# Performance work log

Measured on AMD Instinct MI355X. Metric: run time of the kernel, lower is better.

## Reference

```python
import jax, jax.numpy as jnp
import numpy as np

NEG_INF = -1e30  # large negative in place of -inf for masked scores (fp32-safe)


def setup_inputs() -> dict:
    key = jax.random.key(0)
    kq, kk, kv, km = jax.random.split(key, 4)
    B, H, S, D = 2, 16, 2048, 64
    query = jax.random.normal(kq, (B, H, S, D), dtype=jnp.float32)
    k = jax.random.normal(kk, (B, H, S, D), dtype=jnp.float32)
    v = jax.random.normal(kv, (B, H, S, D), dtype=jnp.float32)
    mask = jax.random.randint(km, (B, H, S, S), 0, 2, dtype=jnp.int32)
    return {"query": query, "key": k, "value": v, "mask": mask}


def reference(query, key, value, mask):
    # Online-softmax chunked attention is mathematically exact softmax attention;
    # we compute the equivalent masked softmax attention in one fused expression.
    d_k = query.shape[-1]
    scale = 1.0 / np.sqrt(d_k).astype(np.float32)
    # scores: [B, H, Sq, Sk]
    scores = jnp.einsum('bhqd,bhkd->bhqk', query, key) * scale
    scores = jnp.where(mask == 0, NEG_INF, scores)
    attn = jax.nn.softmax(scores, axis=-1)
    out = jnp.einsum('bhqk,bhkd->bhqd', attn, value)
    return out
```

## Files before the change

kernel.cpp:

```cpp
#include <hip/hip_runtime.h>


typedef __attribute__((ext_vector_type(8))) short bf16x8;
typedef __attribute__((ext_vector_type(4))) float f32x4;

#define S_LEN 2048
#define D_DIM 64
#define QT 64
#define KT 64
#define LROW 72
#define NEG_BIG (-1e30f)

__device__ __forceinline__ short f2bf(float f) {
    union { float f; unsigned u; } v; v.f = f;
    unsigned r = v.u + 0x7fffu + ((v.u >> 16) & 1u);
    return (short)(r >> 16);
}

__global__ __launch_bounds__(256, 4)
void fa_fwd(const float* __restrict__ Q, const float* __restrict__ K,
            const float* __restrict__ V, const int* __restrict__ M,
            float* __restrict__ O) {
    __shared__ __align__(16) short Kb[KT * LROW];
    __shared__ __align__(16) short Vt[D_DIM * LROW];
    __shared__ __align__(16) short Pw[4 * 16 * LROW];

    const int tid  = threadIdx.x;
    const int lane = tid & 63;
    const int w    = tid >> 6;
    const int quad = lane >> 4;
    const int c    = lane & 15;

    const int bid = blockIdx.x;
    const int x = bid & 7, y = bid >> 3;
    const int bh = x * 4 + (y >> 5);
    const int q0 = (y & 31) * QT;

    const float* qrow = Q + ((size_t)(bh * S_LEN + q0 + w * 16 + c)) * D_DIM;
    bf16x8 qfrag[2];
#pragma unroll
    for (int ks = 0; ks < 2; ++ks) {
        const float* p = qrow + ks * 32 + quad * 8;
        float4 a = *(const float4*)p;
        float4 b = *(const float4*)(p + 4);
        bf16x8 f;
        f[0]=f2bf(a.x); f[1]=f2bf(a.y); f[2]=f2bf(a.z); f[3]=f2bf(a.w);
        f[4]=f2bf(b.x); f[5]=f2bf(b.y); f[6]=f2bf(b.z); f[7]=f2bf(b.w);
        qfrag[ks] = f;
    }

    f32x4 acco[4];
    float m_i[4], l_i[4];
#pragma unroll
    for (int r = 0; r < 4; ++r) {
        m_i[r] = NEG_BIG; l_i[r] = 0.f;
        acco[r][0]=0.f; acco[r][1]=0.f; acco[r][2]=0.f; acco[r][3]=0.f;
    }

    const int kkt = tid >> 2;
    const int dsb = (tid & 3) * 16;
    const int kp  = (tid & 31) * 2;
    const int dbv = (tid >> 5) * 8;
    const float* Kbase = K + (size_t)bh * S_LEN * D_DIM;
    const float* Vbase = V + (size_t)bh * S_LEN * D_DIM;
    const int* mbase = M + ((size_t)(bh * S_LEN + q0 + w * 16 + quad * 4)) * S_LEN + c;
    short* pw = &Pw[w * 16 * LROW];

    for (int k0 = 0; k0 < S_LEN; k0 += KT) {
        int mv[4][4];
#pragma unroll
        for (int reg = 0; reg < 4; ++reg)
#pragma unroll
            for (int nb = 0; nb < 4; ++nb)
                mv[reg][nb] = mbase[(size_t)reg * S_LEN + k0 + nb * 16];

        {
            const float* kr = Kbase + (size_t)(k0 + kkt) * D_DIM + dsb;
            float4 a = *(const float4*)kr;
            float4 b = *(const float4*)(kr + 4);
            float4 cc = *(const float4*)(kr + 8);
            float4 d = *(const float4*)(kr + 12);
            short* dst = &Kb[kkt * LROW + dsb];
            bf16x8 f0, f1;
            f0[0]=f2bf(a.x);  f0[1]=f2bf(a.y);  f0[2]=f2bf(a.z);  f0[3]=f2bf(a.w);
            f0[4]=f2bf(b.x);  f0[5]=f2bf(b.y);  f0[6]=f2bf(b.z);  f0[7]=f2bf(b.w);
            f1[0]=f2bf(cc.x); f1[1]=f2bf(cc.y); f1[2]=f2bf(cc.z); f1[3]=f2bf(cc.w);
            f1[4]=f2bf(d.x);  f1[5]=f2bf(d.y);  f1[6]=f2bf(d.z);  f1[7]=f2bf(d.w);
            *(bf16x8*)dst = f0;
            *(bf16x8*)(dst + 8) = f1;
        }
        {
            const float* v0 = Vbase + (size_t)(k0 + kp) * D_DIM + dbv;
            const float* v1 = v0 + D_DIM;
            float4 a0 = *(const float4*)v0, a1 = *(const float4*)(v0 + 4);
            float4 b0 = *(const float4*)v1, b1 = *(const float4*)(v1 + 4);
            float av[8] = {a0.x,a0.y,a0.z,a0.w,a1.x,a1.y,a1.z,a1.w};
            float bv[8] = {b0.x,b0.y,b0.z,b0.w,b1.x,b1.y,b1.z,b1.w};
#pragma unroll
            for (int i = 0; i < 8; ++i) {
                unsigned pr = (unsigned short)f2bf(av[i]) |
                              ((unsigned)(unsigned short)f2bf(bv[i]) << 16);
                *(unsigned*)&Vt[(dbv + i) * LROW + kp] = pr;
            }
        }
        __syncthreads();

        f32x4 accs[4];
#pragma unroll
        for (int nb = 0; nb < 4; ++nb) { accs[nb][0]=0.f; accs[nb][1]=0.f; accs[nb][2]=0.f; accs[nb][3]=0.f; }
#pragma unroll
        for (int nb = 0; nb < 4; ++nb)
#pragma unroll
            for (int ks = 0; ks < 2; ++ks) {
                bf16x8 bfr = *(const bf16x8*)&Kb[(nb * 16 + c) * LROW + ks * 32 + quad * 8];
                accs[nb] = __builtin_amdgcn_mfma_f32_16x16x32_bf16(qfrag[ks], bfr, accs[nb], 0, 0, 0);
            }

        float s[4][4], rmax[4];
#pragma unroll
        for (int reg = 0; reg < 4; ++reg) {
            float rm = NEG_BIG;
#pragma unroll
            for (int nb = 0; nb < 4; ++nb) {
                float sv = accs[nb][reg] * 0.125f;
                sv = (mv[reg][nb] != 0) ? sv : NEG_BIG;
                s[reg][nb] = sv;
                rm = fmaxf(rm, sv);
            }
            rm = fmaxf(rm, __shfl_xor(rm, 1));
            rm = fmaxf(rm, __shfl_xor(rm, 2));
            rm = fmaxf(rm, __shfl_xor(rm, 4));
            rm = fmaxf(rm, __shfl_xor(rm, 8));
            rmax[reg] = rm;
        }
        float alpha[4];
#pragma unroll
        for (int reg = 0; reg < 4; ++reg) {
            float mn = fmaxf(m_i[reg], rmax[reg]);
            alpha[reg] = __expf(m_i[reg] - mn);
            m_i[reg] = mn;
        }
        float p[4][4];
#pragma unroll
        for (int reg = 0; reg < 4; ++reg) {
            float rs = 0.f;
#pragma unroll
            for (int nb = 0; nb < 4; ++nb) {
                float pv = __expf(s[reg][nb] - m_i[reg]);
                p[reg][nb] = pv;
                rs += pv;
            }
            rs += __shfl_xor(rs, 1);
            rs += __shfl_xor(rs, 2);
            rs += __shfl_xor(rs, 4);
            rs += __shfl_xor(rs, 8);
            l_i[reg] = l_i[reg] * alpha[reg] + rs;
        }
#pragma unroll
        for (int db = 0; db < 4; ++db)
#pragma unroll
            for (int reg = 0; reg < 4; ++reg)
                acco[db][reg] *= alpha[reg];

#pragma unroll
        for (int reg = 0; reg < 4; ++reg)
#pragma unroll
            for (int nb = 0; nb < 4; ++nb)
                pw[(quad * 4 + reg) * LROW + nb * 16 + c] = f2bf(p[reg][nb]);

        bf16x8 pfr0 = *(const bf16x8*)&pw[c * LROW + quad * 8];
        bf16x8 pfr1 = *(const bf16x8*)&pw[c * LROW + 32 + quad * 8];

#pragma unroll
        for (int db = 0; db < 4; ++db) {
            bf16x8 v0f = *(const bf16x8*)&Vt[(db * 16 + c) * LROW + quad * 8];
            acco[db] = __builtin_amdgcn_mfma_f32_16x16x32_bf16(pfr0, v0f, acco[db], 0, 0, 0);
            bf16x8 v1f = *(const bf16x8*)&Vt[(db * 16 + c) * LROW + 32 + quad * 8];
            acco[db] = __builtin_amdgcn_mfma_f32_16x16x32_bf16(pfr1, v1f, acco[db], 0, 0, 0);
        }
        __syncthreads();
    }

    float* orow = O + ((size_t)(bh * S_LEN + q0 + w * 16 + quad * 4)) * D_DIM + c;
#pragma unroll
    for (int reg = 0; reg < 4; ++reg) {
        float inv = 1.0f / l_i[reg];
#pragma unroll
        for (int db = 0; db < 4; ++db)
            orow[(size_t)reg * D_DIM + db * 16] = acco[db][reg] * inv;
    }
}

extern "C" void kernel_launch(void* const* d_in, const int* in_sizes, int n_in,
                              void* d_out, int out_size, void* d_ws, size_t ws_size,
                              hipStream_t stream) {
    const float* Q = (const float*)d_in[0];
    const float* K = (const float*)d_in[1];
    const float* V = (const float*)d_in[2];
    const int*   M = (const int*)d_in[3];
    float* O = (float*)d_out;
    hipLaunchKernelGGL(fa_fwd, dim3(1024), dim3(256), 0, stream, Q, K, V, M, O);
}
```

Measured before the change: 794.2 us.

## Pre-pack Q/K/V into MFMA fragment layout and drop online max rescaling

Adds three pre-pass kernels that convert Q (pre-scaled by 1/8), K and V into bf16 in the exact per-lane MFMA fragment order, stored in workspace. The main kernel then loads K/V tiles straight into LDS with double-buffered global_load_lds while prefetching the mask for the next tile, so per-tile conversion and transposition disappear. It also drops the running max and rescaling and exponentiates raw scores directly, with masked entries set to zero. That removes the shuffles and alpha multiplies but risks overflow for large scores, and a row whose mask is all zero now divides by zero instead of giving the reference's uniform average.

```diff
diff --git a/kernel.cpp b/kernel.cpp
--- a/kernel.cpp
+++ b/kernel.cpp
@@ -6,10 +6,8 @@
 
 #define S_LEN 2048
 #define D_DIM 64
-#define QT 64
-#define KT 64
-#define LROW 72
-#define NEG_BIG (-1e30f)
+#define NT 32
+#define PP 72
 
 __device__ __forceinline__ short f2bf(float f) {
     union { float f; unsigned u; } v; v.f = f;
@@ -17,13 +15,86 @@
     return (short)(r >> 16);
 }
 
-__global__ __launch_bounds__(256, 4)
-void fa_fwd(const float* __restrict__ Q, const float* __restrict__ K,
-            const float* __restrict__ V, const int* __restrict__ M,
-            float* __restrict__ O) {
-    __shared__ __align__(16) short Kb[KT * LROW];
-    __shared__ __align__(16) short Vt[D_DIM * LROW];
-    __shared__ __align__(16) short Pw[4 * 16 * LROW];
+__device__ __forceinline__ bf16x8 cvt8(float4 a, float4 b, float s) {
+    bf16x8 f;
+    f[0]=f2bf(a.x*s); f[1]=f2bf(a.y*s); f[2]=f2bf(a.z*s); f[3]=f2bf(a.w*s);
+    f[4]=f2bf(b.x*s); f[5]=f2bf(b.y*s); f[6]=f2bf(b.z*s); f[7]=f2bf(b.w*s);
+    return f;
+}
+
+__global__ __launch_bounds__(256)
+void pack_q(const float* __restrict__ Q, short* __restrict__ Qw) {
+    const int bh = blockIdx.x, qt = blockIdx.y;
+    for (int ci = threadIdx.x; ci < 512; ci += 256) {
+        int w = ci >> 7, ks = (ci >> 6) & 1, lane = ci & 63;
+        int quad = lane >> 4, c = lane & 15;
+        int row = qt * 64 + w * 16 + c;
+        int d0 = ks * 32 + quad * 8;
+        const float* src = Q + ((size_t)(bh * S_LEN + row)) * D_DIM + d0;
+        float4 a = *(const float4*)src;
+        float4 b = *(const float4*)(src + 4);
+        *(bf16x8*)(Qw + ((size_t)(bh * 32 + qt) * 512 + ci) * 8) = cvt8(a, b, 0.125f);
+    }
+}
+
+__global__ __launch_bounds__(256)
+void pack_k(const float* __restrict__ K, short* __restrict__ Kw) {
+    const int bh = blockIdx.x, t = blockIdx.y;
+    for (int ci = threadIdx.x; ci < 512; ci += 256) {
+        int fb = ci >> 6, lane = ci & 63;
+        int nb = fb >> 1, ks = fb & 1;
+        int quad = lane >> 4, c = lane & 15;
+        int key = t * 64 + c * 4 + nb;
+        int d0 = ks * 32 + quad * 8;
+        const float* src = K + ((size_t)(bh * S_LEN + key)) * D_DIM + d0;
+        float4 a = *(const float4*)src;
+        float4 b = *(const float4*)(src + 4);
+        *(bf16x8*)(Kw + ((size_t)(bh * 32 + t) * 512 + ci) * 8) = cvt8(a, b, 1.0f);
+    }
+}
+
+__global__ __launch_bounds__(256)
+void pack_v(const float* __restrict__ V, short* __restrict__ Vw) {
+    __shared__ float vt[64][65];
+    const int bh = blockIdx.x, t = blockIdx.y;
+    {
+        int key = threadIdx.x >> 2, d0 = (threadIdx.x & 3) * 16;
+        const float* src = V + ((size_t)(bh * S_LEN + t * 64 + key)) * D_DIM + d0;
+        float4 a = *(const float4*)src;
+        float4 b = *(const float4*)(src + 4);
+        float4 cc = *(const float4*)(src + 8);
+        float4 d = *(const float4*)(src + 12);
+        float* dst = &vt[key][d0];
+        dst[0]=a.x; dst[1]=a.y; dst[2]=a.z; dst[3]=a.w;
+        dst[4]=b.x; dst[5]=b.y; dst[6]=b.z; dst[7]=b.w;
+        dst[8]=cc.x; dst[9]=cc.y; dst[10]=cc.z; dst[11]=cc.w;
+        dst[12]=d.x; dst[13]=d.y; dst[14]=d.z; dst[15]=d.w;
+    }
+    __syncthreads();
+    for (int ci = threadIdx.x; ci < 512; ci += 256) {
+        int fb = ci >> 6, lane = ci & 63;
+        int db = fb >> 1, ks = fb & 1;
+        int quad = lane >> 4, c = lane & 15;
+        bf16x8 f;
+#pragma unroll
+        for (int j = 0; j < 8; ++j) {
+            int pos = ks * 32 + quad * 8 + j;
+            int kin = (pos & 15) * 4 + (pos >> 4);
+            f[j] = f2bf(vt[kin][db * 16 + c]);
+        }
+        *(bf16x8*)(Vw + ((size_t)(bh * 32 + t) * 512 + ci) * 8) = f;
+    }
+}
+
+typedef __attribute__((address_space(3))) unsigned lds_u32;
+typedef const __attribute__((address_space(1))) unsigned glob_u32;
+
+__global__ __launch_bounds__(256, 3)
+void fa_main(const short* __restrict__ Qw, const short* __restrict__ Kw,
+             const short* __restrict__ Vw, const int* __restrict__ M,
+             float* __restrict__ O) {
+    __shared__ __align__(16) short KVb[2 * 16 * 512];
+    __shared__ __align__(16) short Pwv[4 * 16 * PP];
 
     const int tid  = threadIdx.x;
     const int lane = tid & 63;
@@ -34,160 +105,111 @@
     const int bid = blockIdx.x;
     const int x = bid & 7, y = bid >> 3;
     const int bh = x * 4 + (y >> 5);
-    const int q0 = (y & 31) * QT;
-
-    const float* qrow = Q + ((size_t)(bh * S_LEN + q0 + w * 16 + c)) * D_DIM;
-    bf16x8 qfrag[2];
-#pragma unroll
-    for (int ks = 0; ks < 2; ++ks) {
-        const float* p = qrow + ks * 32 + quad * 8;
-        float4 a = *(const float4*)p;
-        float4 b = *(const float4*)(p + 4);
-        bf16x8 f;
-        f[0]=f2bf(a.x); f[1]=f2bf(a.y); f[2]=f2bf(a.z); f[3]=f2bf(a.w);
-        f[4]=f2bf(b.x); f[5]=f2bf(b.y); f[6]=f2bf(b.z); f[7]=f2bf(b.w);
-        qfrag[ks] = f;
-    }
+    const int qt = y & 31;
+
+    const short* qbase = Qw + ((size_t)(bh * 32 + qt) * 512 + w * 128 + lane) * 8;
+    const bf16x8 qf0 = *(const bf16x8*)qbase;
+    const bf16x8 qf1 = *(const bf16x8*)(qbase + 64 * 8);
+
+    const short* gkv = (w < 2) ? (Kw + (size_t)bh * 32 * 4096)
+                               : (Vw + (size_t)bh * 32 * 4096);
+    const int fb0 = (w & 1) * 4;
+    const int vofs = (w < 2) ? 0 : 4096;
+
+    const int* mrow = M + ((size_t)(bh * S_LEN + qt * 64 + w * 16 + quad * 4)) * S_LEN + 4 * c;
 
     f32x4 acco[4];
-    float m_i[4], l_i[4];
+    float lacc[4];
 #pragma unroll
     for (int r = 0; r < 4; ++r) {
-        m_i[r] = NEG_BIG; l_i[r] = 0.f;
+        lacc[r] = 0.f;
         acco[r][0]=0.f; acco[r][1]=0.f; acco[r][2]=0.f; acco[r][3]=0.f;
     }
 
-    const int kkt = tid >> 2;
-    const int dsb = (tid & 3) * 16;
-    const int kp  = (tid & 31) * 2;
-    const int dbv = (tid >> 5) * 8;
-    const float* Kbase = K + (size_t)bh * S_LEN * D_DIM;
-    const float* Vbase = V + (size_t)bh * S_LEN * D_DIM;
-    const int* mbase = M + ((size_t)(bh * S_LEN + q0 + w * 16 + quad * 4)) * S_LEN + c;
-    short* pw = &Pw[w * 16 * LROW];
-
-    for (int k0 = 0; k0 < S_LEN; k0 += KT) {
-        int mv[4][4];
-#pragma unroll
-        for (int reg = 0; reg < 4; ++reg)
+#pragma unroll
+    for (int i = 0; i < 4; ++i) {
+        const short* src = gkv + (size_t)(fb0 + i) * 512 + lane * 8;
+        short* dst = &KVb[vofs + (fb0 + i) * 512];
+        __builtin_amdgcn_global_load_lds((glob_u32*)src, (lds_u32*)dst, 16, 0, 0);
+    }
+    int4 mcur[4];
+#pragma unroll
+    for (int r = 0; r < 4; ++r) mcur[r] = *(const int4*)(mrow + (size_t)r * S_LEN);
+    __syncthreads();
+
+    short* pw = &Pwv[w * 16 * PP];
+
+    for (int t = 0; t < NT; ++t) {
+        const int cur = (t & 1) * 8192, nxt = 8192 - cur;
+        const int tn = (t + 1 < NT) ? t + 1 : 0;
+
+#pragma unroll
+        for (int i = 0; i < 4; ++i) {
+            const short* src = gkv + (size_t)tn * 4096 + (fb0 + i) * 512 + lane * 8;
+            short* dst = &KVb[nxt + vofs + (fb0 + i) * 512];
+            __builtin_amdgcn_global_load_lds((glob_u32*)src, (lds_u32*)dst, 16, 0, 0);
+        }
+        int4 mnxt[4];
+#pragma unroll
+        for (int r = 0; r < 4; ++r)
+            mnxt[r] = *(const int4*)(mrow + (size_t)r * S_LEN + tn * 64);
+
+        f32x4 accs[4];
+#pragma unroll
+        for (int nb = 0; nb < 4; ++nb) { accs[nb][0]=0.f; accs[nb][1]=0.f; accs[nb][2]=0.f; accs[nb][3]=0.f; }
+#pragma unroll
+        for (int nb = 0; nb < 4; ++nb) {
+            bf16x8 b0 = *(const bf16x8*)&KVb[cur + (nb * 2 + 0) * 512 + lane * 8];
+            accs[nb] = __builtin_amdgcn_mfma_f32_16x16x32_bf16(qf0, b0, accs[nb], 0, 0, 0);
+            bf16x8 b1 = *(const bf16x8*)&KVb[cur + (nb * 2 + 1) * 512 + lane * 8];
+            accs[nb] = __builtin_amdgcn_mfma_f32_16x16x32_bf16(qf1, b1, accs[nb], 0, 0, 0);
+        }
+
+        float p[4][4];
+#pragma unroll
+        for (int r = 0; r < 4; ++r) {
+            const int mm[4] = { mcur[r].x, mcur[r].y, mcur[r].z, mcur[r].w };
+#pragma unroll
+            for (int nb = 0; nb < 4; ++nb) {
+                float e = __expf(accs[nb][r]);
+                p[r][nb] = (mm[nb] != 0) ? e : 0.f;
+            }
+            lacc[r] += (p[r][0] + p[r][1]) + (p[r][2] + p[r][3]);
+        }
+
+#pragma unroll
+        for (int r = 0; r < 4; ++r)
 #pragma unroll
             for (int nb = 0; nb < 4; ++nb)
-                mv[reg][nb] = mbase[(size_t)reg * S_LEN + k0 + nb * 16];
-
-        {
-            const float* kr = Kbase + (size_t)(k0 + kkt) * D_DIM + dsb;
-            float4 a = *(const float4*)kr;
-            float4 b = *(const float4*)(kr + 4);
-            float4 cc = *(const float4*)(kr + 8);
-            float4 d = *(const float4*)(kr + 12);
-            short* dst = &Kb[kkt * LROW + dsb];
-            bf16x8 f0, f1;
-            f0[0]=f2bf(a.x);  f0[1]=f2bf(a.y);  f0[2]=f2bf(a.z);  f0[3]=f2bf(a.w);
-            f0[4]=f2bf(b.x);  f0[5]=f2bf(b.y);  f0[6]=f2bf(b.z);  f0[7]=f2bf(b.w);
-            f1[0]=f2bf(cc.x); f1[1]=f2bf(cc.y); f1[2]=f2bf(cc.z); f1[3]=f2bf(cc.w);
-            f1[4]=f2bf(d.x);  f1[5]=f2bf(d.y);  f1[6]=f2bf(d.z);  f1[7]=f2bf(d.w);
-            *(bf16x8*)dst = f0;
-            *(bf16x8*)(dst + 8) = f1;
-        }
-        {
-            const float* v0 = Vbase + (size_t)(k0 + kp) * D_DIM + dbv;
-            const float* v1 = v0 + D_DIM;
-            float4 a0 = *(const float4*)v0, a1 = *(const float4*)(v0 + 4);
-            float4 b0 = *(const float4*)v1, b1 = *(const float4*)(v1 + 4);
-            float av[8] = {a0.x,a0.y,a0.z,a0.w,a1.x,a1.y,a1.z,a1.w};
-            float bv[8] = {b0.x,b0.y,b0.z,b0.w,b1.x,b1.y,b1.z,b1.w};
-#pragma unroll
-            for (int i = 0; i < 8; ++i) {
-                unsigned pr = (unsigned short)f2bf(av[i]) |
-                              ((unsigned)(unsigned short)f2bf(bv[i]) << 16);
-                *(unsigned*)&Vt[(dbv + i) * LROW + kp] = pr;
-            }
-        }
+                pw[(quad * 4 + r) * PP + nb * 16 + c] = f2bf(p[r][nb]);
+        bf16x8 pf0 = *(const bf16x8*)&pw[c * PP + quad * 8];
+        bf16x8 pf1 = *(const bf16x8*)&pw[c * PP + 32 + quad * 8];
+
+#pragma unroll
+        for (int db = 0; db < 4; ++db) {
+            bf16x8 v0 = *(const bf16x8*)&KVb[cur + 4096 + (db * 2 + 0) * 512 + lane * 8];
+            acco[db] = __builtin_amdgcn_mfma_f32_16x16x32_bf16(pf0, v0, acco[db], 0, 0, 0);
+            bf16x8 v1 = *(const bf16x8*)&KVb[cur + 4096 + (db * 2 + 1) * 512 + lane * 8];
+            acco[db] = __builtin_amdgcn_mfma_f32_16x16x32_bf16(pf1, v1, acco[db], 0, 0, 0);
+        }
+
+#pragma unroll
+        for (int r = 0; r < 4; ++r) mcur[r] = mnxt[r];
         __syncthreads();
-
-        f32x4 accs[4];
-#pragma unroll
-        for (int nb = 0; nb < 4; ++nb) { accs[nb][0]=0.f; accs[nb][1]=0.f; accs[nb][2]=0.f; accs[nb][3]=0.f; }
-#pragma unroll
-        for (int nb = 0; nb < 4; ++nb)
-#pragma unroll
-            for (int ks = 0; ks < 2; ++ks) {
-                bf16x8 bfr = *(const bf16x8*)&Kb[(nb * 16 + c) * LROW + ks * 32 + quad * 8];
-                accs[nb] = __builtin_amdgcn_mfma_f32_16x16x32_bf16(qfrag[ks], bfr, accs[nb], 0, 0, 0);
-            }
-
-        float s[4][4], rmax[4];
-#pragma unroll
-        for (int reg = 0; reg < 4; ++reg) {
-            float rm = NEG_BIG;
-#pragma unroll
-            for (int nb = 0; nb < 4; ++nb) {
-                float sv = accs[nb][reg] * 0.125f;
-                sv = (mv[reg][nb] != 0) ? sv : NEG_BIG;
-                s[reg][nb] = sv;
-                rm = fmaxf(rm, sv);
-            }
-            rm = fmaxf(rm, __shfl_xor(rm, 1));
-            rm = fmaxf(rm, __shfl_xor(rm, 2));
-            rm = fmaxf(rm, __shfl_xor(rm, 4));
-            rm = fmaxf(rm, __shfl_xor(rm, 8));
-            rmax[reg] = rm;
-        }
-        float alpha[4];
-#pragma unroll
-        for (int reg = 0; reg < 4; ++reg) {
-            float mn = fmaxf(m_i[reg], rmax[reg]);
-            alpha[reg] = __expf(m_i[reg] - mn);
-            m_i[reg] = mn;
-        }
-        float p[4][4];
-#pragma unroll
-        for (int reg = 0; reg < 4; ++reg) {
-            float rs = 0.f;
-#pragma unroll
-            for (int nb = 0; nb < 4; ++nb) {
-                float pv = __expf(s[reg][nb] - m_i[reg]);
-                p[reg][nb] = pv;
-                rs += pv;
-            }
-            rs += __shfl_xor(rs, 1);
-            rs += __shfl_xor(rs, 2);
-            rs += __shfl_xor(rs, 4);
-            rs += __shfl_xor(rs, 8);
-            l_i[reg] = l_i[reg] * alpha[reg] + rs;
-        }
+    }
+
+    float* orow = O + ((size_t)(bh * S_LEN + qt * 64 + w * 16 + quad * 4)) * D_DIM + c;
+#pragma unroll
+    for (int r = 0; r < 4; ++r) {
+        float l = lacc[r];
+        l += __shfl_xor(l, 1);
+        l += __shfl_xor(l, 2);
+        l += __shfl_xor(l, 4);
+        l += __shfl_xor(l, 8);
+        float inv = 1.0f / l;
 #pragma unroll
         for (int db = 0; db < 4; ++db)
-#pragma unroll
-            for (int reg = 0; reg < 4; ++reg)
-                acco[db][reg] *= alpha[reg];
-
-#pragma unroll
-        for (int reg = 0; reg < 4; ++reg)
-#pragma unroll
-            for (int nb = 0; nb < 4; ++nb)
-                pw[(quad * 4 + reg) * LROW + nb * 16 + c] = f2bf(p[reg][nb]);
-
-        bf16x8 pfr0 = *(const bf16x8*)&pw[c * LROW + quad * 8];
-        bf16x8 pfr1 = *(const bf16x8*)&pw[c * LROW + 32 + quad * 8];
-
-#pragma unroll
-        for (int db = 0; db < 4; ++db) {
-            bf16x8 v0f = *(const bf16x8*)&Vt[(db * 16 + c) * LROW + quad * 8];
-            acco[db] = __builtin_amdgcn_mfma_f32_16x16x32_bf16(pfr0, v0f, acco[db], 0, 0, 0);
-            bf16x8 v1f = *(const bf16x8*)&Vt[(db * 16 + c) * LROW + 32 + quad * 8];
-            acco[db] = __builtin_amdgcn_mfma_f32_16x16x32_bf16(pfr1, v1f, acco[db], 0, 0, 0);
-        }
-        __syncthreads();
-    }
-
-    float* orow = O + ((size_t)(bh * S_LEN + q0 + w * 16 + quad * 4)) * D_DIM + c;
-#pragma unroll
-    for (int reg = 0; reg < 4; ++reg) {
-        float inv = 1.0f / l_i[reg];
-#pragma unroll
-        for (int db = 0; db < 4; ++db)
-            orow[(size_t)reg * D_DIM + db * 16] = acco[db][reg] * inv;
+            orow[(size_t)r * D_DIM + db * 16] = acco[db][r] * inv;
     }
 }
 
@@ -199,5 +221,13 @@
     const float* V = (const float*)d_in[2];
     const int*   M = (const int*)d_in[3];
     float* O = (float*)d_out;
-    hipLaunchKernelGGL(fa_fwd, dim3(1024), dim3(256), 0, stream, Q, K, V, M, O);
-}
+
+    short* Qw = (short*)d_ws;
+    short* Kw = Qw + (size_t)32 * 32 * 4096;
+    short* Vw = Kw + (size_t)32 * 32 * 4096;
+
+    hipLaunchKernelGGL(pack_q, dim3(32, 32), dim3(256), 0, stream, Q, Qw);
+    hipLaunchKernelGGL(pack_k, dim3(32, 32), dim3(256), 0, stream, K, Kw);
+    hipLaunchKernelGGL(pack_v, dim3(32, 32), dim3(256), 0, stream, V, Vw);
+    hipLaunchKernelGGL(fa_main, dim3(1024), dim3(256), 0, stream, Qw, Kw, Vw, M, O);
+}
```

Result: no change. 780.4 us (-1.7%).
